# Kernel tuning notes

Hardware: AMD Instinct MI355X
Metric: run time of the kernel (lower is better)

Reference implementation:

```python
import jax, jax.numpy as jnp
import numpy as np

N = 50000          # nodes
E = 1_600_000      # edges (avg degree 32)
IN_CH = 256
HID = 256          # 2 * out_channels
OUT_CH = 128


def setup_inputs() -> dict:
    key = jax.random.key(0)
    k = jax.random.split(key, 5)
    x = jax.random.normal(k[0], (N, IN_CH), dtype=jnp.float32)
    edge_index = jax.random.randint(k[1], (2, E), 0, N, dtype=jnp.int64)
    W1 = jax.random.normal(k[2], (IN_CH, HID), dtype=jnp.float32) * 0.05
    b1 = jnp.zeros((HID,), dtype=jnp.float32)
    W2 = jax.random.normal(k[3], (HID, OUT_CH), dtype=jnp.float32) * 0.05
    b2 = jnp.zeros((OUT_CH,), dtype=jnp.float32)
    return {"x": x, "edge_index": edge_index, "W1": W1, "b1": b1, "W2": W2, "b2": b2}


def _gcn_conv(x, src, dst, deg_inv_sqrt, W, b, n_nodes):
    # GCNConv: linear transform, then normalized sum-aggregation over edges
    # (edge list already includes self-loops; deg_inv_sqrt precomputed).
    h = x @ W                                   # [N, F_out]
    norm = deg_inv_sqrt[src] * deg_inv_sqrt[dst]  # [E+N]
    msg = h[src] * norm[:, None]                # gather + scale
    out = jax.ops.segment_sum(msg, dst, num_segments=n_nodes)  # scatter-add
    return out + b


def reference(x, edge_index, W1, b1, W2, b2):
    n = x.shape[0]
    loop = jnp.arange(n, dtype=edge_index.dtype)
    src = jnp.concatenate([edge_index[0], loop])   # with self-loops
    dst = jnp.concatenate([edge_index[1], loop])
    # symmetric degree normalization (edge weight 1, deg over targets)
    deg = jax.ops.segment_sum(jnp.ones_like(dst, dtype=x.dtype), dst, num_segments=n)
    deg_inv_sqrt = jnp.where(deg > 0, jax.lax.rsqrt(deg), 0.0)

    z = _gcn_conv(x, src, dst, deg_inv_sqrt, W1, b1, n)
    z = jax.nn.relu(z)
    z = _gcn_conv(z, src, dst, deg_inv_sqrt, W2, b2, n)

    # decode: gather endpoint embeddings of original edges, dot product
    value = jnp.sum(z[edge_index[0]] * z[edge_index[1]], axis=-1)  # [E]
    return value.reshape(-1)
```

## Files before the change

### kernel.cpp

```cpp
#include <hip/hip_runtime.h>

#define WS_ALIGN(x) (((x) + 255) & ~(size_t)255)

typedef float f4v __attribute__((ext_vector_type(4)));
__device__ inline void nt_store4(float* p, float4 v) {
  __builtin_nontemporal_store(*(f4v*)&v, (f4v*)p);
}

__global__ void k_count(const int* __restrict__ dst, int E, int* __restrict__ deg) {
  int e = blockIdx.x * blockDim.x + threadIdx.x;
  if (e < E) atomicAdd(&deg[dst[e]], 1);
}

__global__ void k_dis(const int* __restrict__ deg, float* __restrict__ dis, int N) {
  int i = blockIdx.x * blockDim.x + threadIdx.x;
  if (i < N) dis[i] = rsqrtf((float)(deg[i] + 1));
}

__global__ __launch_bounds__(1024) void k_scan(const int* __restrict__ deg,
                                               int* __restrict__ rowptr,
                                               int* __restrict__ cursor,
                                               int N, int Etot) {
  __shared__ int wsum[16];
  __shared__ int s_carry;
  int tid = threadIdx.x, lane = tid & 63, w = tid >> 6;
  if (tid == 0) { s_carry = 0; rowptr[N] = Etot; }
  __syncthreads();
  for (int base = 0; base < N; base += 4096) {
    int i0 = base + tid * 4;
    int v[4];
    #pragma unroll
    for (int u = 0; u < 4; ++u) {
      int i = i0 + u;
      v[u] = (i < N) ? deg[i] : 0;
    }
    int tsum = v[0] + v[1] + v[2] + v[3];
    int sc = tsum;
    #pragma unroll
    for (int off = 1; off < 64; off <<= 1) {
      int t = __shfl_up(sc, off);
      if (lane >= off) sc += t;
    }
    if (lane == 63) wsum[w] = sc;
    __syncthreads();
    if (w == 0 && lane < 16) {
      int xx = wsum[lane];
      #pragma unroll
      for (int off = 1; off < 16; off <<= 1) {
        int t = __shfl_up(xx, off);
        if (lane >= off) xx += t;
      }
      wsum[lane] = xx;
    }
    __syncthreads();
    int woff = (w == 0) ? 0 : wsum[w - 1];
    int excl = s_carry + woff + (sc - tsum);
    #pragma unroll
    for (int u = 0; u < 4; ++u) {
      int i = i0 + u;
      if (i < N) { rowptr[i] = excl; cursor[i] = excl; }
      excl += v[u];
    }
    __syncthreads();
    if (tid == 0) s_carry += wsum[15];
    __syncthreads();
  }
}

__global__ void k_fill_pack(const int* __restrict__ src, const int* __restrict__ dst, int E,
                            int* __restrict__ cursor, unsigned short* __restrict__ csr16,
                            unsigned int* __restrict__ packed) {
  int e = blockIdx.x * blockDim.x + threadIdx.x;
  if (e < E) {
    int s = src[e];
    int d = dst[e];
    packed[e] = (unsigned int)s | ((unsigned int)d << 16);
    int pos = atomicAdd(&cursor[d], 1);
    csr16[pos] = (unsigned short)s;
  }
}

#define BM 128
#define BN 128
#define BK 16
__global__ __launch_bounds__(256) void k_gemm_scale_sm(const float* __restrict__ A,
                                                       const float* __restrict__ B,
                                                       const float* __restrict__ dis,
                                                       float* __restrict__ C,
                                                       int M, int Nc, int K) {
  __shared__ float As[BK][BM];
  __shared__ float Bs[BK][BN];
  int tid = threadIdx.x;
  int block_row = blockIdx.x * BM;
  int block_col = blockIdx.y * BN;
  int tr = (tid >> 4) << 3;
  int tc = (tid & 15) << 3;
  float acc[8][8] = {};
  for (int k0 = 0; k0 < K; k0 += BK) {
    for (int t = tid; t < BM * BK / 4; t += 256) {
      int r = t >> 2;
      int cc = (t & 3) << 2;
      int gr = block_row + r;
      float4 v = {0.f, 0.f, 0.f, 0.f};
      if (gr < M) v = *(const float4*)(A + (size_t)gr * K + k0 + cc);
      As[cc + 0][r] = v.x; As[cc + 1][r] = v.y; As[cc + 2][r] = v.z; As[cc + 3][r] = v.w;
    }
    for (int t = tid; t < BK * BN / 4; t += 256) {
      int r = t >> 5;
      int cc = (t & 31) << 2;
      *(float4*)&Bs[r][cc] = *(const float4*)(B + (size_t)(k0 + r) * Nc + block_col + cc);
    }
    __syncthreads();
    #pragma unroll
    for (int k = 0; k < BK; ++k) {
      float a[8], b[8];
      *(float4*)&a[0] = *(const float4*)&As[k][tr];
      *(float4*)&a[4] = *(const float4*)&As[k][tr + 4];
      *(float4*)&b[0] = *(const float4*)&Bs[k][tc];
      *(float4*)&b[4] = *(const float4*)&Bs[k][tc + 4];
      #pragma unroll
      for (int i = 0; i < 8; ++i)
        #pragma unroll
        for (int j = 0; j < 8; ++j)
          acc[i][j] = fmaf(a[i], b[j], acc[i][j]);
    }
    __syncthreads();
  }
  int col0 = block_col + tc;
  size_t base = ((size_t)(col0 >> 4) * M) * 16 + (col0 & 15);
  for (int i = 0; i < 8; ++i) {
    int gr = block_row + tr + i;
    if (gr >= M) break;
    float s = dis[gr];
    float4 v0 = {acc[i][0] * s, acc[i][1] * s, acc[i][2] * s, acc[i][3] * s};
    float4 v1 = {acc[i][4] * s, acc[i][5] * s, acc[i][6] * s, acc[i][7] * s};
    float* cp = C + base + (size_t)gr * 16;
    *(float4*)cp = v0;
    *(float4*)(cp + 4) = v1;
  }
}

template <int FCH, bool OUTSLICE>
__global__ __launch_bounds__(256) void k_agg_xcd(const float* __restrict__ hs,
                                                 const int* __restrict__ rowptr,
                                                 const unsigned short* __restrict__ csr,
                                                 const float* __restrict__ dis,
                                                 const float* __restrict__ bias,
                                                 float* __restrict__ out,
                                                 int N, int do_relu, int phase) {
  int bid = blockIdx.x;
  int xcd = bid & 7;
  int wid = threadIdx.x >> 6;
  int lane = threadIdx.x & 63;
  int sub = lane >> 3;
  int epar = (lane >> 2) & 1;
  int c2 = lane & 3;
  int wix = ((bid >> 3) << 2) + wid;
  int wpx = ((int)(gridDim.x >> 3)) << 2;
  int nchunk = (N + 7) >> 3;

  int s = xcd + (phase << 3);
  const float* in = hs + (size_t)s * N * 16;
  for (int ch = wix; ch < nchunk; ch += wpx) {
    int node = (ch << 3) + sub;
    bool valid = node < N;
    int b0 = 0, e0 = 0;
    if (valid) { b0 = rowptr[node]; e0 = rowptr[node + 1]; }
    float4 acc = {0.f, 0.f, 0.f, 0.f};
    int j = b0 + epar;
    for (; j + 6 < e0; j += 8) {
      int i0 = csr[j];     int i1 = csr[j + 2];
      int i2 = csr[j + 4]; int i3 = csr[j + 6];
      float4 v0 = *(const float4*)(in + ((size_t)i0 << 4) + (c2 << 2));
      float4 v1 = *(const float4*)(in + ((size_t)i1 << 4) + (c2 << 2));
      float4 v2 = *(const float4*)(in + ((size_t)i2 << 4) + (c2 << 2));
      float4 v3 = *(const float4*)(in + ((size_t)i3 << 4) + (c2 << 2));
      acc.x += (v0.x + v1.x) + (v2.x + v3.x);
      acc.y += (v0.y + v1.y) + (v2.y + v3.y);
      acc.z += (v0.z + v1.z) + (v2.z + v3.z);
      acc.w += (v0.w + v1.w) + (v2.w + v3.w);
    }
    for (; j < e0; j += 2) {
      int idx = csr[j];
      float4 v = *(const float4*)(in + ((size_t)idx << 4) + (c2 << 2));
      acc.x += v.x; acc.y += v.y; acc.z += v.z; acc.w += v.w;
    }
    acc.x += __shfl_xor(acc.x, 4);
    acc.y += __shfl_xor(acc.y, 4);
    acc.z += __shfl_xor(acc.z, 4);
    acc.w += __shfl_xor(acc.w, 4);
    if (valid && epar == 0) {
      float4 self = *(const float4*)(in + ((size_t)node << 4) + (c2 << 2));
      float dn = dis[node];
      int col = (s << 4) + (c2 << 2);
      float4 bv = *(const float4*)(bias + col);
      float4 r;
      r.x = (acc.x + self.x) * dn + bv.x;
      r.y = (acc.y + self.y) * dn + bv.y;
      r.z = (acc.z + self.z) * dn + bv.z;
      r.w = (acc.w + self.w) * dn + bv.w;
      if (do_relu) {
        r.x = fmaxf(r.x, 0.f); r.y = fmaxf(r.y, 0.f);
        r.z = fmaxf(r.z, 0.f); r.w = fmaxf(r.w, 0.f);
      }
      if (OUTSLICE)
        nt_store4(out + (size_t)s * N * 16 + ((size_t)node << 4) + (c2 << 2), r);
      else
        nt_store4(out + (size_t)node * FCH + col, r);
    }
  }
}

__global__ __launch_bounds__(256) void k_decode_xcd4(const float* __restrict__ z,
                                                     const unsigned int* __restrict__ packed,
                                                     float* __restrict__ partial,
                                                     int E, int N) {
  int bid = blockIdx.x;
  int xcd = bid & 7;
  int wid = threadIdx.x >> 6;
  int lane = threadIdx.x & 63;
  int c2 = lane & 3;
  int sub = lane >> 2;
  int wix = ((bid >> 3) << 2) + wid;
  int wpx = ((int)(gridDim.x >> 3)) << 2;
  const float* zc = z + (size_t)xcd * N * 16;
  float* pp = partial + (size_t)xcd * E;

  for (int e0 = wix * 64; e0 < E; e0 += wpx * 64) {
    float pv[4];
    int ev[4];
    #pragma unroll
    for (int q = 0; q < 4; ++q) {
      int e = e0 + q * 16 + sub;
      ev[q] = e;
      pv[q] = 0.f;
      if (e < E) {
        unsigned int pk = packed[e];
        int a = (int)(pk & 0xFFFFu), d = (int)(pk >> 16);
        float4 za = *(const float4*)(zc + ((size_t)a << 4) + (c2 << 2));
        float4 zb = *(const float4*)(zc + ((size_t)d << 4) + (c2 << 2));
        pv[q] = za.x * zb.x + za.y * zb.y + za.z * zb.z + za.w * zb.w;
      }
    }
    #pragma unroll
    for (int q = 0; q < 4; ++q) {
      pv[q] += __shfl_xor(pv[q], 1);
      pv[q] += __shfl_xor(pv[q], 2);
    }
    if (c2 == 0) {
      #pragma unroll
      for (int q = 0; q < 4; ++q)
        if (ev[q] < E) pp[ev[q]] = pv[q];
    }
  }
}

__global__ void k_dreduce4(const float* __restrict__ partial, float* __restrict__ out, int E) {
  int q = blockIdx.x * 256 + threadIdx.x;
  int e = q << 2;
  if (e >= E) return;
  if (e + 4 <= E) {
    float4 s = *(const float4*)(partial + e);
    #pragma unroll
    for (int k = 1; k < 8; ++k) {
      float4 t = *(const float4*)(partial + (size_t)k * E + e);
      s.x += t.x; s.y += t.y; s.z += t.z; s.w += t.w;
    }
    *(float4*)(out + e) = s;
  } else {
    for (int i = e; i < E; ++i) {
      float s = 0.f;
      #pragma unroll
      for (int k = 0; k < 8; ++k) s += partial[(size_t)k * E + i];
      out[i] = s;
    }
  }
}

extern "C" void kernel_launch(void* const* d_in, const int* in_sizes, int n_in,
                              void* d_out, int out_size, void* d_ws, size_t ws_size,
                              hipStream_t stream) {
  const float* x  = (const float*)d_in[0];
  const int* eidx = (const int*)d_in[1];
  const float* W1 = (const float*)d_in[2];
  const float* b1 = (const float*)d_in[3];
  const float* W2 = (const float*)d_in[4];
  const float* b2 = (const float*)d_in[5];
  float* out = (float*)d_out;

  const int IN_CH = 256, HID = 256, OUT_CH = 128;
  const int N = in_sizes[0] / IN_CH;
  const int E = in_sizes[1] / 2;
  const int* esrc = eidx;
  const int* edst = eidx + E;

  char* p = (char*)d_ws;
  auto alloc = [&](size_t bytes) -> char* { char* r = p; p += WS_ALIGN(bytes); return r; };
  int*   deg    = (int*)  alloc(sizeof(int) * N);
  float* dis    = (float*)alloc(sizeof(float) * N);
  int*   rowptr = (int*)  alloc(sizeof(int) * (N + 1));
  int*   cursor = (int*)  alloc(sizeof(int) * N);
  unsigned short* csr16 = (unsigned short*)alloc(sizeof(unsigned short) * (size_t)E);
  unsigned int*   packed = (unsigned int*) alloc(sizeof(unsigned int) * (size_t)E);
  float* bufA   = (float*)alloc(sizeof(float) * (size_t)N * HID);
  float* bufB   = (float*)alloc(sizeof(float) * (size_t)N * HID);

  const int T = 256;
  hipMemsetAsync(deg, 0, sizeof(int) * N, stream);
  hipLaunchKernelGGL(k_count, dim3((E + T - 1) / T), dim3(T), 0, stream, edst, E, deg);
  hipLaunchKernelGGL(k_dis, dim3((N + T - 1) / T), dim3(T), 0, stream, deg, dis, N);
  hipLaunchKernelGGL(k_scan, dim3(1), dim3(1024), 0, stream, deg, rowptr, cursor, N, E);
  hipLaunchKernelGGL(k_fill_pack, dim3((E + T - 1) / T), dim3(T), 0, stream,
                     esrc, edst, E, cursor, csr16, packed);

  const int PG = 2048;

  dim3 g1((N + BM - 1) / BM, HID / BN);
  hipLaunchKernelGGL(k_gemm_scale_sm, g1, dim3(256), 0, stream, x, W1, dis, bufA, N, HID, IN_CH);
  hipLaunchKernelGGL((k_agg_xcd<256, false>), dim3(PG), dim3(256), 0, stream,
                     bufA, rowptr, csr16, dis, b1, bufB, N, 1, 0);
  hipLaunchKernelGGL((k_agg_xcd<256, false>), dim3(PG), dim3(256), 0, stream,
                     bufA, rowptr, csr16, dis, b1, bufB, N, 1, 1);

  dim3 g2((N + BM - 1) / BM, OUT_CH / BN);
  hipLaunchKernelGGL(k_gemm_scale_sm, g2, dim3(256), 0, stream, bufB, W2, dis, bufA, N, OUT_CH, HID);
  hipLaunchKernelGGL((k_agg_xcd<128, true>), dim3(PG), dim3(256), 0, stream,
                     bufA, rowptr, csr16, dis, b2, bufB, N, 0, 0);

  hipLaunchKernelGGL(k_decode_xcd4, dim3(PG), dim3(256), 0, stream,
                     bufB, packed, bufA, E, N);
  hipLaunchKernelGGL(k_dreduce4, dim3((E / 4 + 255) / 256), dim3(256), 0, stream,
                     bufA, out, E);
}
```

Baseline: 765.8 us.

## Move edge packing into count kernel and XCD-partition the CSR fill

Edge packing now happens in the degree-count kernel, so the CSR fill reads one packed 32-bit word per edge instead of separate src and dst arrays. The fill kernel is partitioned by XCD: each of the eight block groups scans every edge but only handles destinations in its own node range. The aim is to keep cursor atomics and csr16 writes local to one XCD's L2. The cost is that each edge is read eight times across the XCD groups.

```diff
diff --git a/kernel.cpp b/kernel.cpp
--- a/kernel.cpp
+++ b/kernel.cpp
@@ -7,9 +7,15 @@
   __builtin_nontemporal_store(*(f4v*)&v, (f4v*)p);
 }
 
-__global__ void k_count(const int* __restrict__ dst, int E, int* __restrict__ deg) {
+__global__ void k_pack_count(const int* __restrict__ src, const int* __restrict__ dst, int E,
+                             unsigned int* __restrict__ packed, int* __restrict__ deg) {
   int e = blockIdx.x * blockDim.x + threadIdx.x;
-  if (e < E) atomicAdd(&deg[dst[e]], 1);
+  if (e < E) {
+    int s = src[e];
+    int d = dst[e];
+    packed[e] = (unsigned int)s | ((unsigned int)d << 16);
+    atomicAdd(&deg[d], 1);
+  }
 }
 
 __global__ void k_dis(const int* __restrict__ deg, float* __restrict__ dis, int N) {
@@ -67,16 +73,23 @@
   }
 }
 
-__global__ void k_fill_pack(const int* __restrict__ src, const int* __restrict__ dst, int E,
-                            int* __restrict__ cursor, unsigned short* __restrict__ csr16,
-                            unsigned int* __restrict__ packed) {
-  int e = blockIdx.x * blockDim.x + threadIdx.x;
-  if (e < E) {
-    int s = src[e];
-    int d = dst[e];
-    packed[e] = (unsigned int)s | ((unsigned int)d << 16);
-    int pos = atomicAdd(&cursor[d], 1);
-    csr16[pos] = (unsigned short)s;
+__global__ __launch_bounds__(256) void k_fill_xcd(const unsigned int* __restrict__ packed,
+                                                  int E, int N,
+                                                  int* __restrict__ cursor,
+                                                  unsigned short* __restrict__ csr16) {
+  int bid = blockIdx.x;
+  int xcd = bid & 7;
+  int tix = ((bid >> 3) << 8) + threadIdx.x;
+  int tpx = ((int)(gridDim.x >> 3)) << 8;
+  int lo = (int)(((long long)N * xcd) >> 3);
+  int hi = (int)(((long long)N * (xcd + 1)) >> 3);
+  for (int e = tix; e < E; e += tpx) {
+    unsigned int pk = packed[e];
+    int d = (int)(pk >> 16);
+    if (d >= lo && d < hi) {
+      int pos = atomicAdd(&cursor[d], 1);
+      csr16[pos] = (unsigned short)(pk & 0xFFFFu);
+    }
   }
 }
 
@@ -306,14 +319,14 @@
   float* bufB   = (float*)alloc(sizeof(float) * (size_t)N * HID);
 
   const int T = 256;
+  const int PG = 2048;
+
   hipMemsetAsync(deg, 0, sizeof(int) * N, stream);
-  hipLaunchKernelGGL(k_count, dim3((E + T - 1) / T), dim3(T), 0, stream, edst, E, deg);
+  hipLaunchKernelGGL(k_pack_count, dim3((E + T - 1) / T), dim3(T), 0, stream,
+                     esrc, edst, E, packed, deg);
   hipLaunchKernelGGL(k_dis, dim3((N + T - 1) / T), dim3(T), 0, stream, deg, dis, N);
   hipLaunchKernelGGL(k_scan, dim3(1), dim3(1024), 0, stream, deg, rowptr, cursor, N, E);
-  hipLaunchKernelGGL(k_fill_pack, dim3((E + T - 1) / T), dim3(T), 0, stream,
-                     esrc, edst, E, cursor, csr16, packed);
-
-  const int PG = 2048;
+  hipLaunchKernelGGL(k_fill_xcd, dim3(PG), dim3(T), 0, stream, packed, E, N, cursor, csr16);
 
   dim3 g1((N + BM - 1) / BM, HID / BN);
   hipLaunchKernelGGL(k_gemm_scale_sm, g1, dim3(256), 0, stream, x, W1, dis, bufA, N, HID, IN_CH);
```

Result: faster. 711.6 us (-7.1%).
